# Optimization experiments

Measured on AMD Instinct MI355X. Metric: run time of the kernel, lower is better.

## Reference

```python
import jax, jax.numpy as jnp
import numpy as np

SHAPES = [(100, 100), (50, 50), (25, 25), (13, 13)]
EMBED, HEADS, LEVELS, POINTS = 256, 8, 4, 4
DH = EMBED // HEADS


def setup_inputs() -> dict:
    key = jax.random.key(0)
    ks = jax.random.split(key, 12)
    bs, nq = 4, 10000
    nv = sum(h * w for h, w in SHAPES)
    s = 0.02
    return {
        'query': jax.random.normal(ks[0], (bs, nq, EMBED), jnp.float32),
        'value': jax.random.normal(ks[1], (bs, nv, EMBED), jnp.float32),
        'reference_points': jax.random.uniform(ks[2], (bs, nq, LEVELS, 2), jnp.float32),
        'spatial_shapes': jnp.array(SHAPES, jnp.int32),
        'Wv': s * jax.random.normal(ks[3], (EMBED, EMBED), jnp.float32),
        'bv': jnp.zeros((EMBED,), jnp.float32),
        'Woff': s * jax.random.normal(ks[4], (EMBED, HEADS * LEVELS * POINTS * 2), jnp.float32),
        'boff': s * jax.random.normal(ks[5], (HEADS * LEVELS * POINTS * 2,), jnp.float32),
        'Ww': s * jax.random.normal(ks[6], (EMBED, HEADS * LEVELS * POINTS), jnp.float32),
        'bw': jnp.zeros((HEADS * LEVELS * POINTS,), jnp.float32),
        'Wo': s * jax.random.normal(ks[7], (EMBED, EMBED), jnp.float32),
        'bo': jnp.zeros((EMBED,), jnp.float32),
    }


def _msda(v, loc, aw, bs, nq):
    # v: (bs, nv, heads, dh); loc: (bs, nq, heads, L, P, 2) normalized in [0,1]
    # aw: (bs, nq, heads, L, P). Bilinear grid_sample, align_corners=False, zero padding.
    out = jnp.zeros((bs, HEADS, nq, DH), v.dtype)
    start = 0
    for l, (H, W) in enumerate(SHAPES):
        vl = v[:, start:start + H * W].transpose(0, 2, 1, 3)  # (bs, heads, H*W, dh)
        start += H * W
        locl = loc[:, :, :, l]                                # (bs, nq, heads, P, 2)
        x = locl[..., 0] * W - 0.5                            # align_corners=False mapping
        y = locl[..., 1] * H - 0.5
        x0 = jnp.floor(x); y0 = jnp.floor(y)
        fx = x - x0; fy = y - y0
        x0i = x0.astype(jnp.int32); y0i = y0.astype(jnp.int32)
        sampled = jnp.zeros((bs, HEADS, nq * POINTS, DH), v.dtype)
        for dy, wy in ((0, 1.0 - fy), (1, fy)):
            for dx, wx in ((0, 1.0 - fx), (1, fx)):
                xi = x0i + dx; yi = y0i + dy
                valid = (xi >= 0) & (xi < W) & (yi >= 0) & (yi < H)
                idx = jnp.clip(yi, 0, W and H - 1) * W + jnp.clip(xi, 0, W - 1)
                idx = jnp.clip(yi, 0, H - 1) * W + jnp.clip(xi, 0, W - 1)
                idx_t = idx.transpose(0, 2, 1, 3).reshape(bs, HEADS, nq * POINTS)
                g = jnp.take_along_axis(vl, idx_t[..., None], axis=2)  # (bs,heads,nq*P,dh)
                w = jnp.where(valid, wx * wy, 0.0).transpose(0, 2, 1, 3).reshape(bs, HEADS, -1)
                sampled = sampled + g * w[..., None]
        awl = aw[:, :, :, l].transpose(0, 2, 1, 3).reshape(bs, HEADS, nq * POINTS)
        out = out + (sampled * awl[..., None]).reshape(bs, HEADS, nq, POINTS, DH).sum(3)
    return out.transpose(0, 2, 1, 3).reshape(bs, nq, EMBED)


def reference(query, value, reference_points, spatial_shapes, Wv, bv, Woff, boff, Ww, bw, Wo, bo):
    bs, nq, _ = query.shape
    v = (value @ Wv + bv).reshape(bs, -1, HEADS, DH)
    off = (query @ Woff + boff).reshape(bs, nq, HEADS, LEVELS, POINTS, 2)
    aw = jax.nn.softmax((query @ Ww + bw).reshape(bs, nq, HEADS, LEVELS * POINTS), axis=-1)
    aw = aw.reshape(bs, nq, HEADS, LEVELS, POINTS)
    normalizer = jnp.stack([spatial_shapes[:, 1], spatial_shapes[:, 0]], -1).astype(query.dtype)  # (L,2) = (W,H)
    loc = reference_points[:, :, None, :, None, :] + off / normalizer[None, None, None, :, None, :]
    out = _msda(v, loc, aw, bs, nq)
    out = out @ Wo + bo
    return out + query  # identity residual (dropout in eval mode)
```

## Files before the change

### kernel.cpp

```cpp
#include <hip/hip_runtime.h>
#include <hip/hip_bf16.h>

#define BS     4
#define NQ     10000
#define NV     13294
#define EMBED  256
#define HEADS  8
#define LEVELS 4
#define POINTS 4
#define DH     32

typedef __attribute__((ext_vector_type(8))) short short8;
typedef __attribute__((ext_vector_type(4))) float floatx4;

static __device__ __forceinline__ unsigned short f2b(float f) {
    __hip_bfloat16 h = __float2bfloat16(f);
    return *(unsigned short*)&h;
}
static __device__ __forceinline__ float b2f(unsigned short u) {
    return __uint_as_float(((unsigned int)u) << 16);
}
static __device__ __forceinline__ unsigned int pk_bf16(float x, float y) {
    __hip_bfloat162 h = __float22bfloat162_rn(make_float2(x, y));
    unsigned int u; __builtin_memcpy(&u, &h, 4); return u;
}

__global__ __launch_bounds__(256) void prep_weights(
    const float* __restrict__ Wv,  const float* __restrict__ Woff,
    const float* __restrict__ boff,const float* __restrict__ Ww,
    const float* __restrict__ bw,  const float* __restrict__ Wo,
    unsigned short* __restrict__ Wvt, unsigned short* __restrict__ Wcatt,
    unsigned short* __restrict__ Wot, float* __restrict__ bcat)
{
    const int n = blockIdx.x;
    const int k = threadIdx.x;
    if (n < 256) {
        Wvt[n * 256 + k] = f2b(Wv[k * 256 + n]);
    } else if (n < 512) {
        Wcatt[(n - 256) * 256 + k] = f2b(Woff[k * 256 + (n - 256)]);
    } else if (n < 640) {
        Wcatt[(n - 256) * 256 + k] = f2b(Ww[k * 128 + (n - 512)]);
    } else {
        Wot[(n - 640) * 256 + k] = f2b(Wo[k * 256 + (n - 640)]);
    }
    if (n == 0) {
        for (int j = k; j < 384; j += 256)
            bcat[j] = (j < 256) ? boff[j] : bw[j - 256];
    }
}

#define ASTR 72

template<int MODE, bool AF32>
static __device__ __forceinline__ void gemm_body(
    unsigned short* As, unsigned short* Bsh,
    const void* __restrict__ Aptr, int M,
    const unsigned short* __restrict__ Bt,
    const float* __restrict__ bias,
    void* __restrict__ Cv, int ldc,
    const float* __restrict__ residual,
    int mb, int nb)
{
    const int t  = threadIdx.x;
    const int m0 = mb * 128;
    const int n0 = nb * 128;
    const int K  = 256;

    const int wv   = t >> 6;
    const int lane = t & 63;
    const int wm   = (wv & 1) * 64;
    const int wn   = (wv >> 1) * 64;
    const int lr   = lane & 15;
    const int lk   = (lane >> 4) * 8;

    floatx4 acc[4][4] = {};

    const int ar = t >> 1;
    const int ac = (t & 1) * 32;

    for (int k0 = 0; k0 < K; k0 += 64) {
        uint4 a[4] = {{}, {}, {}, {}};
        const int arow = m0 + ar;
        if (AF32) {
            if (arow < M) {
                const float4* s = (const float4*)((const float*)Aptr + (size_t)arow * K + k0 + ac);
                #pragma unroll
                for (int i = 0; i < 4; ++i) {
                    const float4 f0 = s[2 * i], f1 = s[2 * i + 1];
                    a[i].x = pk_bf16(f0.x, f0.y);
                    a[i].y = pk_bf16(f0.z, f0.w);
                    a[i].z = pk_bf16(f1.x, f1.y);
                    a[i].w = pk_bf16(f1.z, f1.w);
                }
            }
        } else {
            if (arow < M) {
                const uint4* s = (const uint4*)((const unsigned short*)Aptr + (size_t)arow * K + k0 + ac);
                a[0] = s[0]; a[1] = s[1]; a[2] = s[2]; a[3] = s[3];
            }
        }
        const uint4* bs = (const uint4*)(Bt + (size_t)(n0 + ar) * K + k0 + ac);
        const uint4 b0 = bs[0], b1 = bs[1], b2 = bs[2], b3 = bs[3];

        __syncthreads();
        {
            uint4* ad = (uint4*)&As[ar * ASTR + ac];
            ad[0] = a[0]; ad[1] = a[1]; ad[2] = a[2]; ad[3] = a[3];
            uint4* bd = (uint4*)&Bsh[ar * ASTR + ac];
            bd[0] = b0; bd[1] = b1; bd[2] = b2; bd[3] = b3;
        }
        __syncthreads();

        #pragma unroll
        for (int kk = 0; kk < 64; kk += 32) {
            short8 bf[4];
            #pragma unroll
            for (int nt = 0; nt < 4; ++nt)
                bf[nt] = *(const short8*)&Bsh[(wn + nt * 16 + lr) * ASTR + kk + lk];
            #pragma unroll
            for (int mt = 0; mt < 4; ++mt) {
                const short8 af = *(const short8*)&As[(wm + mt * 16 + lr) * ASTR + kk + lk];
                #pragma unroll
                for (int nt = 0; nt < 4; ++nt)
                    acc[mt][nt] = __builtin_amdgcn_mfma_f32_16x16x32_bf16(af, bf[nt], acc[mt][nt], 0, 0, 0);
            }
        }
    }

    const int rbase = m0 + wm + (lane >> 4) * 4;
    #pragma unroll
    for (int nt = 0; nt < 4; ++nt) {
        const int col = n0 + wn + nt * 16 + lr;
        const float bb = bias[col];
        #pragma unroll
        for (int mt = 0; mt < 4; ++mt) {
            #pragma unroll
            for (int r = 0; r < 4; ++r) {
                const int row = rbase + mt * 16 + r;
                if (row < M) {
                    float val = acc[mt][nt][r] + bb;
                    if (MODE == 2) val += residual[(size_t)row * ldc + col];
                    if (MODE == 0)
                        ((unsigned short*)Cv)[(size_t)row * ldc + col] = f2b(val);
                    else
                        ((float*)Cv)[(size_t)row * ldc + col] = val;
                }
            }
        }
    }
}

__global__ __launch_bounds__(256) void gemm_fused12(
    const float* __restrict__ value, const float* __restrict__ query,
    const unsigned short* __restrict__ Wvt, const unsigned short* __restrict__ Wcatt,
    const float* __restrict__ bv, const float* __restrict__ bcat,
    unsigned short* __restrict__ vout, unsigned short* __restrict__ projout)
{
    __shared__ __align__(16) unsigned short As[128 * ASTR];
    __shared__ __align__(16) unsigned short Bsh[128 * ASTR];
    const unsigned int bid = blockIdx.x;
    if (bid < 832u) {
        gemm_body<0, true>(As, Bsh, value, BS * NV, Wvt, bv, vout, 256, nullptr,
                           (int)(bid >> 1), (int)(bid & 1));
    } else {
        const unsigned int b2 = bid - 832u;
        gemm_body<0, true>(As, Bsh, query, BS * NQ, Wcatt, bcat, projout, 384, nullptr,
                           (int)(b2 / 3u), (int)(b2 % 3u));
    }
}

__global__ __launch_bounds__(256) void gemm_out(
    const unsigned short* __restrict__ msda, const unsigned short* __restrict__ Wot,
    const float* __restrict__ bo, float* __restrict__ out,
    const float* __restrict__ query)
{
    __shared__ __align__(16) unsigned short As[128 * ASTR];
    __shared__ __align__(16) unsigned short Bsh[128 * ASTR];
    gemm_body<2, false>(As, Bsh, msda, BS * NQ, Wot, bo, out, 256, query,
                        (int)blockIdx.x, (int)blockIdx.y);
}

__global__ __launch_bounds__(256) void msda_sample(
    const unsigned short* __restrict__ v,
    const unsigned short* __restrict__ proj,
    const float* __restrict__ rp,
    unsigned short* __restrict__ out)
{
    __shared__ __align__(16) unsigned int taps[4 * 1056];

    const int wave = threadIdx.x >> 6;
    const int lane = threadIdx.x & 63;
    const int q = blockIdx.x * 4 + wave;
    const int b = blockIdx.y;
    const int rowq = b * NQ + q;
    const unsigned short* prow = proj + (size_t)rowq * 384;

    const int hA = lane >> 3;
    const int li = lane & 7;
    const int c0 = li * 2;

    const ushort2 lgu = *(const ushort2*)&prow[256 + hA * 16 + c0];
    const float lgx = b2f(lgu.x), lgy = b2f(lgu.y);
    float mx = fmaxf(lgx, lgy);
    mx = fmaxf(mx, __shfl_xor(mx, 1));
    mx = fmaxf(mx, __shfl_xor(mx, 2));
    mx = fmaxf(mx, __shfl_xor(mx, 4));
    const float e0 = __expf(lgx - mx);
    const float e1 = __expf(lgy - mx);
    float ssum = e0 + e1;
    ssum += __shfl_xor(ssum, 1);
    ssum += __shfl_xor(ssum, 2);
    ssum += __shfl_xor(ssum, 4);
    const float inv = 1.0f / ssum;

    const int l = c0 >> 2;
    const int Wl = (l == 0) ? 100 : (l == 1) ? 50 : (l == 2) ? 25 : 13;
    const int st = (l == 0) ? 0 : (l == 1) ? 10000 : (l == 2) ? 12500 : 13125;
    const int Hl = Wl;
    const float fW = (float)Wl, fH = (float)Hl;

    const float2 rxy = *(const float2*)&rp[((size_t)rowq * 4 + l) * 2];

    unsigned int* tbase = taps + wave * 1056 + hA * 132;

    #pragma unroll
    for (int cc = 0; cc < 2; ++cc) {
        const int c = c0 + cc;
        const ushort2 oxyu = *(const ushort2*)&prow[hA * 32 + c * 2];
        const float ox = b2f(oxyu.x), oy = b2f(oxyu.y);
        const float aww = (cc ? e1 : e0) * inv;
        const float x = fmaf(rxy.x, fW, ox) - 0.5f;
        const float y = fmaf(rxy.y, fH, oy) - 0.5f;
        const float x0f = floorf(x), y0f = floorf(y);
        const float fx = x - x0f, fy = y - y0f;
        const int ix = (int)x0f, iy = (int)y0f;
        const float wxv[2] = {1.f - fx, fx};
        const float wyv[2] = {1.f - fy, fy};

        uint4 ent[2];
        #pragma unroll
        for (int tp = 0; tp < 4; ++tp) {
            const int dy = tp >> 1, dx = tp & 1;
            const int xi = ix + dx, yi = iy + dy;
            const bool ok = (xi >= 0) && (xi < Wl) && (yi >= 0) && (yi < Hl);
            const int cx = min(max(xi, 0), Wl - 1);
            const int cy = min(max(yi, 0), Hl - 1);
            const unsigned int off = (unsigned int)(st + cy * Wl + cx) * 512u + (unsigned int)hA * 64u;
            const float w = ok ? wyv[dy] * wxv[dx] * aww : 0.f;
            ((unsigned int*)&ent[tp >> 1])[(tp & 1) * 2 + 0] = off;
            ((unsigned int*)&ent[tp >> 1])[(tp & 1) * 2 + 1] = __float_as_uint(w);
        }
        *(uint4*)&tbase[(c * 4 + 0) * 2] = ent[0];
        *(uint4*)&tbase[(c * 4 + 2) * 2] = ent[1];
    }

    __syncthreads();

    const int h = lane >> 3;
    const unsigned int lane_off = (unsigned int)(lane & 7) * 8u;
    const char* vbase = (const char*)v + (size_t)b * NV * 512;
    const uint4* tp4 = (const uint4*)(taps + wave * 1056 + h * 132);

    float a0 = 0.f, a1 = 0.f, a2 = 0.f, a3 = 0.f;
    #pragma unroll 8
    for (int j = 0; j < 32; ++j) {
        const uint4 ee = tp4[j];
        const uint2 g0 = *(const uint2*)(vbase + (ee.x + lane_off));
        const uint2 g1 = *(const uint2*)(vbase + (ee.z + lane_off));
        const float w0 = __uint_as_float(ee.y);
        const float w1 = __uint_as_float(ee.w);
        a0 = fmaf(w0, __uint_as_float(g0.x << 16), a0);
        a1 = fmaf(w0, __uint_as_float(g0.x & 0xFFFF0000u), a1);
        a2 = fmaf(w0, __uint_as_float(g0.y << 16), a2);
        a3 = fmaf(w0, __uint_as_float(g0.y & 0xFFFF0000u), a3);
        a0 = fmaf(w1, __uint_as_float(g1.x << 16), a0);
        a1 = fmaf(w1, __uint_as_float(g1.x & 0xFFFF0000u), a1);
        a2 = fmaf(w1, __uint_as_float(g1.y << 16), a2);
        a3 = fmaf(w1, __uint_as_float(g1.y & 0xFFFF0000u), a3);
    }

    ushort4 o;
    o.x = f2b(a0); o.y = f2b(a1); o.z = f2b(a2); o.w = f2b(a3);
    *(ushort4*)&out[(size_t)rowq * 256 + h * 32 + (lane & 7) * 4] = o;
}

extern "C" void kernel_launch(void* const* d_in, const int* in_sizes, int n_in,
                              void* d_out, int out_size, void* d_ws, size_t ws_size,
                              hipStream_t stream) {
    const float* query = (const float*)d_in[0];
    const float* value = (const float*)d_in[1];
    const float* rp    = (const float*)d_in[2];
    const float* Wv    = (const float*)d_in[4];
    const float* bv    = (const float*)d_in[5];
    const float* Woff  = (const float*)d_in[6];
    const float* boff  = (const float*)d_in[7];
    const float* Ww    = (const float*)d_in[8];
    const float* bw    = (const float*)d_in[9];
    const float* Wo    = (const float*)d_in[10];
    const float* bo    = (const float*)d_in[11];
    float* out = (float*)d_out;

    const int Mv = BS * NV;
    const int Mq = BS * NQ;

    char* ws = (char*)d_ws;
    const size_t SZ_MSDA = (size_t)Mq * 256 * 2;
    const size_t SZ_V    = (size_t)Mv * 256 * 2;
    const size_t SZ_PROJ = (size_t)Mq * 384 * 2;
    unsigned short* msda  = (unsigned short*)(ws);
    unsigned short* v_bf  = (unsigned short*)(ws + SZ_MSDA);
    unsigned short* proj  = (unsigned short*)(ws + SZ_MSDA + SZ_V);
    char* wp = ws + SZ_MSDA + SZ_V + SZ_PROJ;
    unsigned short* Wvt   = (unsigned short*)(wp);
    unsigned short* Wcatt = (unsigned short*)(wp + 256 * 256 * 2);
    unsigned short* Wot   = (unsigned short*)(wp + 256 * 256 * 2 + 384 * 256 * 2);
    float*          bcat  = (float*)(wp + 256 * 256 * 2 + 384 * 256 * 2 + 256 * 256 * 2);

    prep_weights<<<896, 256, 0, stream>>>(Wv, Woff, boff, Ww, bw, Wo, Wvt, Wcatt, Wot, bcat);

    gemm_fused12<<<832 + 939, 256, 0, stream>>>(
        value, query, Wvt, Wcatt, bv, bcat, v_bf, proj);

    msda_sample<<<dim3(NQ / 4, BS), 256, 0, stream>>>(v_bf, proj, rp, msda);

    gemm_out<<<dim3((Mq + 127) / 128, 2), 256, 0, stream>>>(msda, Wot, bo, out, query);
}
```

Before: 331.6 us.

## Pre-convert GEMM inputs to bf16 and stage tiles via direct global-to-LDS loads

```diff
diff --git a/kernel.cpp b/kernel.cpp
--- a/kernel.cpp
+++ b/kernel.cpp
@@ -10,6 +10,9 @@
 #define POINTS 4
 #define DH     32
 
+#define MV_PAD 53248
+#define MQ_PAD 40064
+
 typedef __attribute__((ext_vector_type(8))) short short8;
 typedef __attribute__((ext_vector_type(4))) float floatx4;
 
@@ -25,89 +28,95 @@
     unsigned int u; __builtin_memcpy(&u, &h, 4); return u;
 }
 
-__global__ __launch_bounds__(256) void prep_weights(
+static __device__ __forceinline__ void gload_lds16(const unsigned short* g, unsigned short* l) {
+    __builtin_amdgcn_global_load_lds(
+        (const __attribute__((address_space(1))) void*)g,
+        (__attribute__((address_space(3))) void*)l,
+        16, 0, 0);
+}
+
+#define CONV_BLOCKS 2048
+
+__global__ __launch_bounds__(256) void prep_convert(
     const float* __restrict__ Wv,  const float* __restrict__ Woff,
     const float* __restrict__ boff,const float* __restrict__ Ww,
     const float* __restrict__ bw,  const float* __restrict__ Wo,
+    const float* __restrict__ value, const float* __restrict__ query,
     unsigned short* __restrict__ Wvt, unsigned short* __restrict__ Wcatt,
-    unsigned short* __restrict__ Wot, float* __restrict__ bcat)
+    unsigned short* __restrict__ Wot, float* __restrict__ bcat,
+    unsigned short* __restrict__ v16, unsigned short* __restrict__ q16)
 {
     const int n = blockIdx.x;
     const int k = threadIdx.x;
-    if (n < 256) {
-        Wvt[n * 256 + k] = f2b(Wv[k * 256 + n]);
-    } else if (n < 512) {
-        Wcatt[(n - 256) * 256 + k] = f2b(Woff[k * 256 + (n - 256)]);
-    } else if (n < 640) {
-        Wcatt[(n - 256) * 256 + k] = f2b(Ww[k * 128 + (n - 512)]);
-    } else {
-        Wot[(n - 640) * 256 + k] = f2b(Wo[k * 256 + (n - 640)]);
-    }
-    if (n == 0) {
-        for (int j = k; j < 384; j += 256)
-            bcat[j] = (j < 256) ? boff[j] : bw[j - 256];
-    }
-}
-
-#define ASTR 72
-
-template<int MODE, bool AF32>
+    if (n < 896) {
+        if (n < 256) {
+            Wvt[n * 256 + k] = f2b(Wv[k * 256 + n]);
+        } else if (n < 512) {
+            Wcatt[(n - 256) * 256 + k] = f2b(Woff[k * 256 + (n - 256)]);
+        } else if (n < 640) {
+            Wcatt[(n - 256) * 256 + k] = f2b(Ww[k * 128 + (n - 512)]);
+        } else {
+            Wot[(n - 640) * 256 + k] = f2b(Wo[k * 256 + (n - 640)]);
+        }
+        if (n == 0) {
+            for (int j = k; j < 384; j += 256)
+                bcat[j] = (j < 256) ? boff[j] : bw[j - 256];
+        }
+        return;
+    }
+    const long long NV8 = (long long)BS * NV * 256 / 8;
+    const long long NQ8 = (long long)BS * NQ * 256 / 8;
+    const long long stride = (long long)CONV_BLOCKS * 256;
+    for (long long u = (long long)(n - 896) * 256 + k; u < NV8 + NQ8; u += stride) {
+        const float4* s;
+        unsigned short* d;
+        if (u < NV8) { s = (const float4*)value + u * 2;         d = v16 + u * 8; }
+        else         { s = (const float4*)query + (u - NV8) * 2; d = q16 + (u - NV8) * 8; }
+        const float4 f0 = s[0], f1 = s[1];
+        uint4 o;
+        o.x = pk_bf16(f0.x, f0.y);
+        o.y = pk_bf16(f0.z, f0.w);
+        o.z = pk_bf16(f1.x, f1.y);
+        o.w = pk_bf16(f1.z, f1.w);
+        *(uint4*)d = o;
+    }
+}
+
+template<int MODE>
 static __device__ __forceinline__ void gemm_body(
-    unsigned short* As, unsigned short* Bsh,
-    const void* __restrict__ Aptr, int M,
+    unsigned short* As, unsigned short* Bs,
+    const unsigned short* __restrict__ A, int M,
     const unsigned short* __restrict__ Bt,
     const float* __restrict__ bias,
     void* __restrict__ Cv, int ldc,
     const float* __restrict__ residual,
     int mb, int nb)
 {
-    const int t  = threadIdx.x;
+    const int t    = threadIdx.x;
+    const int w    = t >> 6;
+    const int lane = t & 63;
     const int m0 = mb * 128;
     const int n0 = nb * 128;
-    const int K  = 256;
-
-    const int wv   = t >> 6;
-    const int lane = t & 63;
-    const int wm   = (wv & 1) * 64;
-    const int wn   = (wv >> 1) * 64;
-    const int lr   = lane & 15;
-    const int lk   = (lane >> 4) * 8;
+    const int wm = (w & 1) * 64;
+    const int wn = (w >> 1) * 64;
+    const int lr = lane & 15;
+    const int lk = (lane >> 4) * 8;
+
+    const int srow = w * 8 + (lane >> 3);
+    const int scol = ((lane & 7) ^ (lane >> 3)) * 8;
+    const unsigned short* ga = A  + (size_t)(m0 + srow) * 256 + scol;
+    const unsigned short* gb = Bt + (size_t)(n0 + srow) * 256 + scol;
+    unsigned short* lA = As + w * 512;
+    unsigned short* lB = Bs + w * 512;
 
     floatx4 acc[4][4] = {};
 
-    const int ar = t >> 1;
-    const int ac = (t & 1) * 32;
-
-    for (int k0 = 0; k0 < K; k0 += 64) {
-        uint4 a[4] = {{}, {}, {}, {}};
-        const int arow = m0 + ar;
-        if (AF32) {
-            if (arow < M) {
-                const float4* s = (const float4*)((const float*)Aptr + (size_t)arow * K + k0 + ac);
-                #pragma unroll
-                for (int i = 0; i < 4; ++i) {
-                    const float4 f0 = s[2 * i], f1 = s[2 * i + 1];
-                    a[i].x = pk_bf16(f0.x, f0.y);
-                    a[i].y = pk_bf16(f0.z, f0.w);
-                    a[i].z = pk_bf16(f1.x, f1.y);
-                    a[i].w = pk_bf16(f1.z, f1.w);
-                }
-            }
-        } else {
-            if (arow < M) {
-                const uint4* s = (const uint4*)((const unsigned short*)Aptr + (size_t)arow * K + k0 + ac);
-                a[0] = s[0]; a[1] = s[1]; a[2] = s[2]; a[3] = s[3];
-            }
-        }
-        const uint4* bs = (const uint4*)(Bt + (size_t)(n0 + ar) * K + k0 + ac);
-        const uint4 b0 = bs[0], b1 = bs[1], b2 = bs[2], b3 = bs[3];
-
+    for (int k0 = 0; k0 < 256; k0 += 64) {
         __syncthreads();
-        {
-            uint4* ad = (uint4*)&As[ar * ASTR + ac];
-            ad[0] = a[0]; ad[1] = a[1]; ad[2] = a[2]; ad[3] = a[3];
-            uint4* bd = (uint4*)&Bsh[ar * ASTR + ac];
-            bd[0] = b0; bd[1] = b1; bd[2] = b2; bd[3] = b3;
+        #pragma unroll
+        for (int j = 0; j < 4; ++j) {
+            gload_lds16(ga + (size_t)j * 32 * 256 + k0, lA + j * 2048);
+            gload_lds16(gb + (size_t)j * 32 * 256 + k0, lB + j * 2048);
         }
         __syncthreads();
 
@@ -115,11 +124,16 @@
         for (int kk = 0; kk < 64; kk += 32) {
             short8 bf[4];
             #pragma unroll
-            for (int nt = 0; nt < 4; ++nt)
-                bf[nt] = *(const short8*)&Bsh[(wn + nt * 16 + lr) * ASTR + kk + lk];
+            for (int nt = 0; nt < 4; ++nt) {
+                const int row = wn + nt * 16 + lr;
+                const int cb  = ((kk + lk) * 2) ^ ((row & 7) << 4);
+                bf[nt] = *(const short8*)((const char*)Bs + row * 128 + cb);
+            }
             #pragma unroll
             for (int mt = 0; mt < 4; ++mt) {
-                const short8 af = *(const short8*)&As[(wm + mt * 16 + lr) * ASTR + kk + lk];
+                const int row = wm + mt * 16 + lr;
+                const int cb  = ((kk + lk) * 2) ^ ((row & 7) << 4);
+                const short8 af = *(const short8*)((const char*)As + row * 128 + cb);
                 #pragma unroll
                 for (int nt = 0; nt < 4; ++nt)
                     acc[mt][nt] = __builtin_amdgcn_mfma_f32_16x16x32_bf16(af, bf[nt], acc[mt][nt], 0, 0, 0);
@@ -131,14 +145,14 @@
     #pragma unroll
     for (int nt = 0; nt < 4; ++nt) {
         const int col = n0 + wn + nt * 16 + lr;
-        const float bb = bias[col];
+        const float bb_ = bias[col];
         #pragma unroll
         for (int mt = 0; mt < 4; ++mt) {
             #pragma unroll
             for (int r = 0; r < 4; ++r) {
                 const int row = rbase + mt * 16 + r;
                 if (row < M) {
-                    float val = acc[mt][nt][r] + bb;
+                    float val = acc[mt][nt][r] + bb_;
                     if (MODE == 2) val += residual[(size_t)row * ldc + col];
                     if (MODE == 0)
                         ((unsigned short*)Cv)[(size_t)row * ldc + col] = f2b(val);
@@ -151,21 +165,21 @@
 }
 
 __global__ __launch_bounds__(256) void gemm_fused12(
-    const float* __restrict__ value, const float* __restrict__ query,
+    const unsigned short* __restrict__ v16, const unsigned short* __restrict__ q16,
     const unsigned short* __restrict__ Wvt, const unsigned short* __restrict__ Wcatt,
     const float* __restrict__ bv, const float* __restrict__ bcat,
     unsigned short* __restrict__ vout, unsigned short* __restrict__ projout)
 {
-    __shared__ __align__(16) unsigned short As[128 * ASTR];
-    __shared__ __align__(16) unsigned short Bsh[128 * ASTR];
+    __shared__ __align__(16) unsigned short As[128 * 64];
+    __shared__ __align__(16) unsigned short Bs[128 * 64];
     const unsigned int bid = blockIdx.x;
     if (bid < 832u) {
-        gemm_body<0, true>(As, Bsh, value, BS * NV, Wvt, bv, vout, 256, nullptr,
-                           (int)(bid >> 1), (int)(bid & 1));
+        gemm_body<0>(As, Bs, v16, BS * NV, Wvt, bv, vout, 256, nullptr,
+                     (int)(bid >> 1), (int)(bid & 1));
     } else {
         const unsigned int b2 = bid - 832u;
-        gemm_body<0, true>(As, Bsh, query, BS * NQ, Wcatt, bcat, projout, 384, nullptr,
-                           (int)(b2 / 3u), (int)(b2 % 3u));
+        gemm_body<0>(As, Bs, q16, BS * NQ, Wcatt, bcat, projout, 384, nullptr,
+                     (int)(b2 / 3u), (int)(b2 % 3u));
     }
 }
 
@@ -174,10 +188,10 @@
     const float* __restrict__ bo, float* __restrict__ out,
     const float* __restrict__ query)
 {
-    __shared__ __align__(16) unsigned short As[128 * ASTR];
-    __shared__ __align__(16) unsigned short Bsh[128 * ASTR];
-    gemm_body<2, false>(As, Bsh, msda, BS * NQ, Wot, bo, out, 256, query,
-                        (int)blockIdx.x, (int)blockIdx.y);
+    __shared__ __align__(16) unsigned short As[128 * 64];
+    __shared__ __align__(16) unsigned short Bs[128 * 64];
+    gemm_body<2>(As, Bs, msda, BS * NQ, Wot, bo, out, 256, query,
+                 (int)blockIdx.x, (int)blockIdx.y);
 }
 
 __global__ __launch_bounds__(256) void msda_sample(
@@ -300,28 +314,34 @@
     const float* bo    = (const float*)d_in[11];
     float* out = (float*)d_out;
 
-    const int Mv = BS * NV;
     const int Mq = BS * NQ;
 
     char* ws = (char*)d_ws;
-    const size_t SZ_MSDA = (size_t)Mq * 256 * 2;
-    const size_t SZ_V    = (size_t)Mv * 256 * 2;
+    const size_t SZ_MSDA = (size_t)MQ_PAD * 256 * 2;
+    const size_t SZ_VIN  = (size_t)MV_PAD * 256 * 2;
+    const size_t SZ_QIN  = (size_t)MQ_PAD * 256 * 2;
+    const size_t SZ_VPR  = (size_t)BS * NV * 256 * 2;
     const size_t SZ_PROJ = (size_t)Mq * 384 * 2;
+
     unsigned short* msda  = (unsigned short*)(ws);
-    unsigned short* v_bf  = (unsigned short*)(ws + SZ_MSDA);
-    unsigned short* proj  = (unsigned short*)(ws + SZ_MSDA + SZ_V);
-    char* wp = ws + SZ_MSDA + SZ_V + SZ_PROJ;
+    unsigned short* v16   = (unsigned short*)(ws + SZ_MSDA);
+    unsigned short* q16   = (unsigned short*)(ws + SZ_MSDA + SZ_VIN);
+    unsigned short* v_prj = (unsigned short*)(ws + SZ_MSDA + SZ_VIN + SZ_QIN);
+    unsigned short* proj  = (unsigned short*)(ws + SZ_MSDA + SZ_VIN + SZ_QIN + SZ_VPR);
+    char* wp = ws + SZ_MSDA + SZ_VIN + SZ_QIN + SZ_VPR + SZ_PROJ;
     unsigned short* Wvt   = (unsigned short*)(wp);
     unsigned short* Wcatt = (unsigned short*)(wp + 256 * 256 * 2);
     unsigned short* Wot   = (unsigned short*)(wp + 256 * 256 * 2 + 384 * 256 * 2);
     float*          bcat  = (float*)(wp + 256 * 256 * 2 + 384 * 256 * 2 + 256 * 256 * 2);
 
-    prep_weights<<<896, 256, 0, stream>>>(Wv, Woff, boff, Ww, bw, Wo, Wvt, Wcatt, Wot, bcat);
+    prep_convert<<<896 + CONV_BLOCKS, 256, 0, stream>>>(
+        Wv, Woff, boff, Ww, bw, Wo, value, query,
+        Wvt, Wcatt, Wot, bcat, v16, q16);
 
     gemm_fused12<<<832 + 939, 256, 0, stream>>>(
-        value, query, Wvt, Wcatt, bv, bcat, v_bf, proj);
-
-    msda_sample<<<dim3(NQ / 4, BS), 256, 0, stream>>>(v_bf, proj, rp, msda);
+        v16, q16, Wvt, Wcatt, bv, bcat, v_prj, proj);
+
+    msda_sample<<<dim3(NQ / 4, BS), 256, 0, stream>>>(v_prj, proj, rp, msda);
 
     gemm_out<<<dim3((Mq + 127) / 128, 2), 256, 0, stream>>>(msda, Wot, bo, out, query);
 }
```

Result: faster. 319.3 us (-3.7%).
